# Kernel tuning notes

Measured on AMD Instinct MI355X. Metric: run time of the kernel, lower is better.

Reference implementation:

```python
import jax, jax.numpy as jnp
import numpy as np

BW_MIN, BW_MAX, FLOAT_AMT, NEG_SLOPE = 0.1, 0.5, 0.1, 0.1


def setup_inputs() -> dict:
    key = jax.random.key(0)
    ks = jax.random.split(key, 24)
    B, S, IN_CH, GRID_CH, IC, DIR, OUT_CH = 8, 2000, 120, 64, 512, 4, 2
    NUM_BLOCK = 8
    n_layers = NUM_BLOCK - 2  # 6
    # grid coordinates: meshgrid over [0,10) with gap 0.1 -> 100x100 = 10000 pts
    gx = np.arange(0.0, 10.0, 0.1)
    gy = np.arange(0.0, 10.0, 0.1)
    GX, GY = np.meshgrid(gx, gy)
    grid_coors_xy = jnp.asarray(np.stack([GX.flatten(), GY.flatten()], axis=1), dtype=jnp.float32)  # [N,2]
    N = grid_coors_xy.shape[0]
    cat_ch = IN_CH + 2 * GRID_CH  # 248
    inp = {
        'input_stuff': jax.random.normal(ks[0], (B, S, IN_CH), jnp.float32),
        'sound_loc': jax.random.uniform(ks[1], (B, 4), jnp.float32) * 10.0,  # inside grid extent
        'grid_coors_xy': grid_coors_xy,
        'xy_offset': jnp.zeros((N, 2), jnp.float32),
        'bandwidths': jnp.full((N,), 0.25, jnp.float32),
        'grid_0': jax.random.normal(ks[2], (N, GRID_CH), jnp.float32) / np.sqrt(float(GRID_CH)),
        'proj_W': jax.random.normal(ks[3], (cat_ch, IC), jnp.float32) / np.sqrt(float(cat_ch)),
        'proj_b': jnp.zeros((IC,), jnp.float32),
        'res_W0': jax.random.normal(ks[4], (cat_ch, IC), jnp.float32) / np.sqrt(float(cat_ch)),
        'res_b0': jnp.zeros((IC,), jnp.float32),
        'res_W1': jax.random.normal(ks[5], (IC, IC), jnp.float32) / np.sqrt(float(IC)),
        'res_b1': jnp.zeros((IC,), jnp.float32),
        'layers_W': jax.random.normal(ks[6], (n_layers, IC, IC), jnp.float32) / np.sqrt(float(IC)),
        'layers_b': jnp.zeros((n_layers, IC), jnp.float32),
        'channels': jax.random.normal(ks[7], (NUM_BLOCK - 1, DIR, IC), jnp.float32) / np.sqrt(float(IC)),
        'out_W': jax.random.normal(ks[8], (IC, OUT_CH), jnp.float32) / np.sqrt(float(IC)),
        'out_b': jnp.zeros((OUT_CH,), jnp.float32),
    }
    return inp


def _leaky(x):
    return jax.nn.leaky_relu(x, NEG_SLOPE)


def _fit_predict(grid_pos, grid_feat, query_pos, bandwidths):
    d2 = jnp.sum((query_pos[:, None, :] - grid_pos[None, :, :]) ** 2, axis=-1)  # [B,N]
    w = jnp.exp(-d2 / (bandwidths[None, :] ** 2))                               # [B,N]
    w = w / jnp.sum(w, axis=-1, keepdims=True)
    return w @ grid_feat                                                        # [B,F]


def reference(input_stuff, sound_loc, grid_coors_xy, xy_offset, bandwidths, grid_0,
              proj_W, proj_b, res_W0, res_b0, res_W1, res_b1,
              layers_W, layers_b, channels, out_W, out_b):
    B, S = input_stuff.shape[0], input_stuff.shape[1]
    bw = jnp.clip(bandwidths, BW_MIN, BW_MAX)
    grid_baseline = grid_coors_xy + jnp.tanh(xy_offset) * FLOAT_AMT
    feat0 = _fit_predict(grid_baseline, grid_0, sound_loc[:, :2], bw)  # [B,64]
    feat1 = _fit_predict(grid_baseline, grid_0, sound_loc[:, 2:], bw)  # [B,64]
    total_grid = jnp.concatenate([feat0, feat1], axis=-1)              # [B,128]
    total_grid = jnp.broadcast_to(total_grid[:, None, :], (B, S, total_grid.shape[-1]))
    my_input = jnp.concatenate([total_grid, input_stuff], axis=-1)     # [B,S,248]

    # proj then broadcast over direction channels + learned channel embedding
    out = (my_input @ proj_W + proj_b)[:, :, None, :] + channels[0][None, None]  # [B,S,4,512]

    n_layers = layers_W.shape[0]
    half = n_layers // 2 - 1
    for k in range(n_layers):
        out = _leaky(out) @ layers_W[k] + layers_b[k] + channels[k + 1][None, None]
        if k == half:
            r = _leaky(my_input @ res_W0 + res_b0) @ res_W1 + res_b1  # [B,S,512]
            out = out + r[:, :, None, :]
    return out @ out_W + out_b  # [B,S,4,2]
```

## Files before the change

### kernel.cpp

```cpp
#include <hip/hip_runtime.h>
#include <hip/hip_bf16.h>

#define BB 8
#define SS 2000
#define IN_CH 120
#define GRID_CH 64
#define NPTS 10000
#define IC 512
#define DIRS 4
#define CATCH 248
#define CATPAD 256
#define NLAY 6
#define MROWS 16000
#define MROWS4 64000
#define NSLICE 16
#define PTS_PER_SLICE 625

typedef __bf16 bf16x8 __attribute__((ext_vector_type(8)));
typedef float f32x4 __attribute__((ext_vector_type(4)));

#define DEVI __device__ __forceinline__

DEVI unsigned short f2bf(float f) {
    __hip_bfloat16 h = __float2bfloat16(f);
    return __builtin_bit_cast(unsigned short, h);
}
DEVI float bf2f(unsigned short u) {
    unsigned int x = ((unsigned int)u) << 16;
    return __builtin_bit_cast(float, x);
}
DEVI float leaky(float x) { return x > 0.f ? x : 0.1f * x; }

DEVI void gload16(const void* g, void* l) {
    __builtin_amdgcn_global_load_lds(
        (const unsigned int __attribute__((address_space(1)))*)g,
        (unsigned int __attribute__((address_space(3)))*)l, 16, 0, 0);
}

DEVI int xcd_swizzle() {
    int nwg = (int)gridDim.x;
    int orig = (int)blockIdx.x;
    int q = nwg >> 3, r = nwg & 7;
    int xcd = orig & 7, pos = orig >> 3;
    int base = xcd < r ? xcd * (q + 1) : r * (q + 1) + (xcd - r) * q;
    return base + pos;
}

static const size_t OFF_FEATS  = 0;
static const size_t OFF_PROJWT = 4096;
static const size_t OFF_RES0WT = 266240;
static const size_t OFF_RES1WT = 528384;
static const size_t OFF_LAYWT  = 1052672;
static const size_t OFF_MYIN   = 4198400;
static const size_t OFF_R0     = 12390400;
static const size_t OFF_R      = 28774400;
static const size_t OFF_A0     = 45158400;
static const size_t OFF_A1     = 110694400;

__global__ void wconv_k(const float* __restrict__ src, unsigned short* __restrict__ dst,
                        int K, int Kpad, int N, int total) {
    int idx = blockIdx.x * 256 + threadIdx.x;
    if (idx >= total) return;
    int k = idx % Kpad;
    int rem = idx / Kpad;
    int n = rem % N;
    int l = rem / N;
    float v = (k < K) ? src[((size_t)l * K + k) * N + n] : 0.f;
    dst[idx] = f2bf(v);
}

__global__ __launch_bounds__(256) void feats_part_k(
    const float* __restrict__ gxy, const float* __restrict__ goff,
    const float* __restrict__ bws, const float* __restrict__ g0,
    const float* __restrict__ sloc, float* __restrict__ partial) {
    int bq = blockIdx.x;
    int b = bq >> 1, q = bq & 1;
    float qx = sloc[b * 4 + q * 2 + 0];
    float qy = sloc[b * 4 + q * 2 + 1];
    int i0 = blockIdx.y * PTS_PER_SLICE;
    int iend = i0 + PTS_PER_SLICE;
    float swt = 0.f;
    float sf[64];
#pragma unroll
    for (int c = 0; c < 64; c++) sf[c] = 0.f;
    for (int i = i0 + threadIdx.x; i < iend; i += 256) {
        float gx = gxy[i * 2 + 0] + tanhf(goff[i * 2 + 0]) * 0.1f;
        float gy = gxy[i * 2 + 1] + tanhf(goff[i * 2 + 1]) * 0.1f;
        float bw = fminf(fmaxf(bws[i], 0.1f), 0.5f);
        float dx = qx - gx, dy = qy - gy;
        float w = expf(-(dx * dx + dy * dy) / (bw * bw));
        swt += w;
#pragma unroll
        for (int c = 0; c < 64; c++) sf[c] += w * g0[(size_t)i * 64 + c];
    }
#pragma unroll
    for (int c = 0; c < 64; c++)
        for (int o = 32; o; o >>= 1) sf[c] += __shfl_down(sf[c], o);
    for (int o = 32; o; o >>= 1) swt += __shfl_down(swt, o);
    __shared__ float red[4][65];
    int lane = threadIdx.x & 63, wv = threadIdx.x >> 6;
    if (lane == 0) {
#pragma unroll
        for (int c = 0; c < 64; c++) red[wv][c] = sf[c];
        red[wv][64] = swt;
    }
    __syncthreads();
    size_t base = (size_t)(blockIdx.y * 16 + bq) * 72;
    if (threadIdx.x < 64) {
        int c = threadIdx.x;
        partial[base + c] = red[0][c] + red[1][c] + red[2][c] + red[3][c];
        if (c == 0)
            partial[base + 64] = red[0][64] + red[1][64] + red[2][64] + red[3][64];
    }
}

__global__ __launch_bounds__(128) void feats_reduce_k(
    const float* __restrict__ partial, float* __restrict__ feats) {
    int bq = blockIdx.x;
    __shared__ float s[66];
    int t = threadIdx.x;
    if (t < 65) {
        float acc = 0.f;
        for (int sl = 0; sl < NSLICE; ++sl)
            acc += partial[(size_t)(sl * 16 + bq) * 72 + t];
        s[t] = acc;
    }
    __syncthreads();
    if (t < 64) {
        int b = bq >> 1, q = bq & 1;
        feats[b * 128 + q * 64 + t] = s[t] / s[64];
    }
}

__global__ void build_k(const float* __restrict__ feats, const float* __restrict__ inp,
                        unsigned short* __restrict__ dst) {
    int idx = blockIdx.x * 256 + threadIdx.x;
    int c = idx & 255;
    int m = idx >> 8;
    int b = m / SS;
    float v;
    if (c < 128) v = feats[b * 128 + c];
    else if (c < CATCH) v = inp[(size_t)m * IN_CH + (c - 128)];
    else v = 0.f;
    dst[idx] = f2bf(v);
}

template <int EPI>
__global__ __launch_bounds__(256) void gemm_k(
    const unsigned short* __restrict__ A, const unsigned short* __restrict__ BT,
    unsigned short* __restrict__ out, int K,
    const float* __restrict__ bias, const float* __restrict__ chan,
    const unsigned short* __restrict__ resid) {
    __shared__ __align__(16) unsigned short lds[2][2][8192];
    const int tid = threadIdx.x;
    const int lane = tid & 63, wv = tid >> 6;
    const int wm = wv >> 1, wn = wv & 1;
    const int c8 = lane >> 4;
    const int fr = lane & 15;

    const int swz = xcd_swizzle();
    const int bx = swz >> 2, by = swz & 3;

    int aoff[4][2], boff[4][2];
#pragma unroll
    for (int i = 0; i < 4; i++) {
        int ra = wm * 64 + i * 16 + fr;
        int rb = wn * 64 + i * 16 + fr;
#pragma unroll
        for (int h = 0; h < 2; h++) {
            int c = c8 + h * 4;
            aoff[i][h] = ra * 64 + ((c ^ (ra & 7)) << 3);
            boff[i][h] = rb * 64 + ((c ^ (rb & 7)) << 3);
        }
    }
    int ldso[4];
    size_t asrc[4];
    const unsigned short* Ab = A + (size_t)bx * 128 * K;
    const unsigned short* Bb = BT + (size_t)by * 128 * K;
#pragma unroll
    for (int t = 0; t < 4; t++) {
        int o = t * 4096 + wv * 1024 + lane * 16;
        int r = o >> 7;
        int s = (o >> 4) & 7;
        int g = (s ^ (r & 7)) << 3;
        ldso[t] = o >> 1;
        asrc[t] = (size_t)r * K + g;
    }

    f32x4 acc[4][4];
#pragma unroll
    for (int i = 0; i < 4; i++)
#pragma unroll
        for (int j = 0; j < 4; j++) acc[i][j] = (f32x4)0.f;

    const int nK = K >> 6;
#pragma unroll
    for (int t = 0; t < 4; t++) gload16(Ab + asrc[t], &lds[0][0][ldso[t]]);
#pragma unroll
    for (int t = 0; t < 4; t++) gload16(Bb + asrc[t], &lds[0][1][ldso[t]]);
    asm volatile("s_waitcnt vmcnt(0)" ::: "memory");
    __builtin_amdgcn_s_barrier();
    __builtin_amdgcn_sched_barrier(0);

    int buf = 0;
    for (int kt = 0; kt < nK; ++kt) {
        if (kt + 1 < nK) {
            const int k1 = (kt + 1) << 6;
#pragma unroll
            for (int t = 0; t < 4; t++) gload16(Ab + asrc[t] + k1, &lds[buf ^ 1][0][ldso[t]]);
#pragma unroll
            for (int t = 0; t < 4; t++) gload16(Bb + asrc[t] + k1, &lds[buf ^ 1][1][ldso[t]]);
        }
#pragma unroll
        for (int h = 0; h < 2; h++) {
            bf16x8 av[4], bv[4];
#pragma unroll
            for (int i = 0; i < 4; i++) av[i] = *(const bf16x8*)&lds[buf][0][aoff[i][h]];
#pragma unroll
            for (int j = 0; j < 4; j++) bv[j] = *(const bf16x8*)&lds[buf][1][boff[j][h]];
#pragma unroll
            for (int i = 0; i < 4; i++)
#pragma unroll
                for (int j = 0; j < 4; j++)
                    acc[i][j] = __builtin_amdgcn_mfma_f32_16x16x32_bf16(av[i], bv[j], acc[i][j], 0, 0, 0);
        }
        if (kt + 1 < nK) {
            asm volatile("s_waitcnt vmcnt(0)" ::: "memory");
            __builtin_amdgcn_s_barrier();
            __builtin_amdgcn_sched_barrier(0);
        }
        buf ^= 1;
    }

    const int rbase = (lane >> 4) << 2;
    const size_t m0 = (size_t)bx * 128;
    const int n0 = by * 128;
#pragma unroll
    for (int i = 0; i < 4; i++) {
#pragma unroll
        for (int j = 0; j < 4; j++) {
#pragma unroll
            for (int rg = 0; rg < 4; ++rg) {
                size_t m = m0 + wm * 64 + i * 16 + rbase + rg;
                int n = n0 + wn * 64 + j * 16 + fr;
                float v = acc[i][j][rg];
                if constexpr (EPI == 0) {
                    float v0 = v + bias[n];
#pragma unroll
                    for (int d = 0; d < 4; ++d) {
                        float u = v0 + chan[d * 512 + n];
                        out[(m * 4 + d) * 512 + n] = f2bf(leaky(u));
                    }
                } else if constexpr (EPI == 1 || EPI == 2 || EPI == 3) {
                    int d = (int)(m & 3);
                    float u = v + bias[n] + chan[d * 512 + n];
                    if constexpr (EPI == 2) u += bf2f(resid[(m >> 2) * 512 + n]);
                    out[m * 512 + n] = f2bf(EPI == 3 ? u : leaky(u));
                } else {
                    float u = v + bias[n];
                    out[m * 512 + n] = f2bf(EPI == 4 ? leaky(u) : u);
                }
            }
        }
    }
}

__global__ __launch_bounds__(256) void final_k(
    const unsigned short* __restrict__ A, const float* __restrict__ outW,
    const float* __restrict__ outb, float* __restrict__ out) {
    int gw = blockIdx.x * 4 + (threadIdx.x >> 6);
    int lane = threadIdx.x & 63;
    const unsigned short* row = A + (size_t)gw * 512;
    uint4 bits = *(const uint4*)(row + lane * 8);
    unsigned int ww[4] = {bits.x, bits.y, bits.z, bits.w};
    float s0 = 0.f, s1 = 0.f;
#pragma unroll
    for (int j = 0; j < 8; j++) {
        unsigned short u = (unsigned short)((ww[j >> 1] >> ((j & 1) * 16)) & 0xffff);
        float a = bf2f(u);
        int k = lane * 8 + j;
        s0 = fmaf(a, outW[k * 2 + 0], s0);
        s1 = fmaf(a, outW[k * 2 + 1], s1);
    }
    for (int o = 32; o; o >>= 1) {
        s0 += __shfl_down(s0, o);
        s1 += __shfl_down(s1, o);
    }
    if (lane == 0) {
        out[(size_t)gw * 2 + 0] = s0 + outb[0];
        out[(size_t)gw * 2 + 1] = s1 + outb[1];
    }
}

extern "C" void kernel_launch(void* const* d_in, const int* in_sizes, int n_in,
                              void* d_out, int out_size, void* d_ws, size_t ws_size,
                              hipStream_t stream) {
    const float* input_stuff = (const float*)d_in[0];
    const float* sound_loc   = (const float*)d_in[1];
    const float* grid_xy     = (const float*)d_in[2];
    const float* xy_offset   = (const float*)d_in[3];
    const float* bandwidths  = (const float*)d_in[4];
    const float* grid_0      = (const float*)d_in[5];
    const float* proj_W      = (const float*)d_in[6];
    const float* proj_b      = (const float*)d_in[7];
    const float* res_W0      = (const float*)d_in[8];
    const float* res_b0      = (const float*)d_in[9];
    const float* res_W1      = (const float*)d_in[10];
    const float* res_b1      = (const float*)d_in[11];
    const float* layers_W    = (const float*)d_in[12];
    const float* layers_b    = (const float*)d_in[13];
    const float* channels    = (const float*)d_in[14];
    const float* out_W       = (const float*)d_in[15];
    const float* out_b       = (const float*)d_in[16];

    char* ws = (char*)d_ws;
    float* feats            = (float*)(ws + OFF_FEATS);
    unsigned short* projWT  = (unsigned short*)(ws + OFF_PROJWT);
    unsigned short* res0WT  = (unsigned short*)(ws + OFF_RES0WT);
    unsigned short* res1WT  = (unsigned short*)(ws + OFF_RES1WT);
    unsigned short* layWT   = (unsigned short*)(ws + OFF_LAYWT);
    unsigned short* myin    = (unsigned short*)(ws + OFF_MYIN);
    unsigned short* R0      = (unsigned short*)(ws + OFF_R0);
    unsigned short* Rb      = (unsigned short*)(ws + OFF_R);
    unsigned short* A0      = (unsigned short*)(ws + OFF_A0);
    unsigned short* A1      = (unsigned short*)(ws + OFF_A1);
    float* partial          = (float*)(ws + OFF_A0);

    wconv_k<<<(512 * 256 + 255) / 256, 256, 0, stream>>>(proj_W, projWT, CATCH, CATPAD, IC, 512 * 256);
    wconv_k<<<(512 * 256 + 255) / 256, 256, 0, stream>>>(res_W0, res0WT, CATCH, CATPAD, IC, 512 * 256);
    wconv_k<<<(512 * 512 + 255) / 256, 256, 0, stream>>>(res_W1, res1WT, IC, IC, IC, 512 * 512);
    wconv_k<<<(6 * 512 * 512 + 255) / 256, 256, 0, stream>>>(layers_W, layWT, IC, IC, IC, 6 * 512 * 512);

    feats_part_k<<<dim3(16, NSLICE), 256, 0, stream>>>(grid_xy, xy_offset, bandwidths, grid_0, sound_loc, partial);
    feats_reduce_k<<<16, 128, 0, stream>>>(partial, feats);
    build_k<<<MROWS, 256, 0, stream>>>(feats, input_stuff, myin);

    gemm_k<0><<<500, 256, 0, stream>>>(myin, projWT, A0, CATPAD, proj_b, channels, nullptr);
    gemm_k<4><<<500, 256, 0, stream>>>(myin, res0WT, R0, CATPAD, res_b0, nullptr, nullptr);
    gemm_k<5><<<500, 256, 0, stream>>>(R0, res1WT, Rb, IC, res_b1, nullptr, nullptr);
    gemm_k<1><<<2000, 256, 0, stream>>>(A0, layWT + 0 * 262144, A1, IC, layers_b + 0 * 512, channels + 1 * 2048, nullptr);
    gemm_k<1><<<2000, 256, 0, stream>>>(A1, layWT + 1 * 262144, A0, IC, layers_b + 1 * 512, channels + 2 * 2048, nullptr);
    gemm_k<2><<<2000, 256, 0, stream>>>(A0, layWT + 2 * 262144, A1, IC, layers_b + 2 * 512, channels + 3 * 2048, Rb);
    gemm_k<1><<<2000, 256, 0, stream>>>(A1, layWT + 3 * 262144, A0, IC, layers_b + 3 * 512, channels + 4 * 2048, nullptr);
    gemm_k<1><<<2000, 256, 0, stream>>>(A0, layWT + 4 * 262144, A1, IC, layers_b + 4 * 512, channels + 5 * 2048, nullptr);
    gemm_k<3><<<2000, 256, 0, stream>>>(A1, layWT + 5 * 262144, A0, IC, layers_b + 5 * 512, channels + 6 * 2048, nullptr);

    final_k<<<MROWS, 256, 0, stream>>>(A0, out_W, out_b, (float*)d_out);
}
```

Baseline: 403.8 us.

## Halve GEMM K-tile to 32 with k-chunk-major LDS layout and higher occupancy

Shrinks the GEMM K-step from 64 to 32, halving LDS from 64KB to 32KB per block. The LDS layout changes from row-major with XOR swizzle to k-chunk-major, so fragment reads need no swizzle. Launch bounds now request 4 blocks per CU to improve latency hiding. In exchange there are twice as many K iterations and barriers, and each sync has less MFMA work to hide global load latency behind.

```diff
diff --git a/kernel.cpp b/kernel.cpp
--- a/kernel.cpp
+++ b/kernel.cpp
@@ -4,13 +4,10 @@
 #define BB 8
 #define SS 2000
 #define IN_CH 120
-#define GRID_CH 64
 #define NPTS 10000
 #define IC 512
-#define DIRS 4
 #define CATCH 248
 #define CATPAD 256
-#define NLAY 6
 #define MROWS 16000
 #define MROWS4 64000
 #define NSLICE 16
@@ -146,12 +143,12 @@
 }
 
 template <int EPI>
-__global__ __launch_bounds__(256) void gemm_k(
+__global__ __launch_bounds__(256, 4) void gemm_k(
     const unsigned short* __restrict__ A, const unsigned short* __restrict__ BT,
     unsigned short* __restrict__ out, int K,
     const float* __restrict__ bias, const float* __restrict__ chan,
     const unsigned short* __restrict__ resid) {
-    __shared__ __align__(16) unsigned short lds[2][2][8192];
+    __shared__ __align__(16) unsigned short lds[2][2][4096];
     const int tid = threadIdx.x;
     const int lane = tid & 63, wv = tid >> 6;
     const int wm = wv >> 1, wn = wv & 1;
@@ -161,30 +158,23 @@
     const int swz = xcd_swizzle();
     const int bx = swz >> 2, by = swz & 3;
 
-    int aoff[4][2], boff[4][2];
+    int aoff[4], boff[4];
 #pragma unroll
     for (int i = 0; i < 4; i++) {
-        int ra = wm * 64 + i * 16 + fr;
-        int rb = wn * 64 + i * 16 + fr;
-#pragma unroll
-        for (int h = 0; h < 2; h++) {
-            int c = c8 + h * 4;
-            aoff[i][h] = ra * 64 + ((c ^ (ra & 7)) << 3);
-            boff[i][h] = rb * 64 + ((c ^ (rb & 7)) << 3);
-        }
-    }
-    int ldso[4];
-    size_t asrc[4];
+        aoff[i] = c8 * 1024 + (wm * 64 + i * 16 + fr) * 8;
+        boff[i] = c8 * 1024 + (wn * 64 + i * 16 + fr) * 8;
+    }
+    int ldso[2];
+    size_t src[2];
     const unsigned short* Ab = A + (size_t)bx * 128 * K;
     const unsigned short* Bb = BT + (size_t)by * 128 * K;
 #pragma unroll
-    for (int t = 0; t < 4; t++) {
-        int o = t * 4096 + wv * 1024 + lane * 16;
-        int r = o >> 7;
-        int s = (o >> 4) & 7;
-        int g = (s ^ (r & 7)) << 3;
+    for (int t = 0; t < 2; t++) {
+        int o = t * 4096 + tid * 16;
+        int ck = o >> 11;
+        int r = (o >> 4) & 127;
         ldso[t] = o >> 1;
-        asrc[t] = (size_t)r * K + g;
+        src[t] = (size_t)r * K + ck * 8;
     }
 
     f32x4 acc[4][4];
@@ -193,11 +183,11 @@
 #pragma unroll
         for (int j = 0; j < 4; j++) acc[i][j] = (f32x4)0.f;
 
-    const int nK = K >> 6;
-#pragma unroll
-    for (int t = 0; t < 4; t++) gload16(Ab + asrc[t], &lds[0][0][ldso[t]]);
-#pragma unroll
-    for (int t = 0; t < 4; t++) gload16(Bb + asrc[t], &lds[0][1][ldso[t]]);
+    const int nK = K >> 5;
+#pragma unroll
+    for (int t = 0; t < 2; t++) gload16(Ab + src[t], &lds[0][0][ldso[t]]);
+#pragma unroll
+    for (int t = 0; t < 2; t++) gload16(Bb + src[t], &lds[0][1][ldso[t]]);
     asm volatile("s_waitcnt vmcnt(0)" ::: "memory");
     __builtin_amdgcn_s_barrier();
     __builtin_amdgcn_sched_barrier(0);
@@ -205,25 +195,22 @@
     int buf = 0;
     for (int kt = 0; kt < nK; ++kt) {
         if (kt + 1 < nK) {
-            const int k1 = (kt + 1) << 6;
-#pragma unroll
-            for (int t = 0; t < 4; t++) gload16(Ab + asrc[t] + k1, &lds[buf ^ 1][0][ldso[t]]);
-#pragma unroll
-            for (int t = 0; t < 4; t++) gload16(Bb + asrc[t] + k1, &lds[buf ^ 1][1][ldso[t]]);
+            const int k1 = (kt + 1) << 5;
+#pragma unroll
+            for (int t = 0; t < 2; t++) gload16(Ab + src[t] + k1, &lds[buf ^ 1][0][ldso[t]]);
+#pragma unroll
+            for (int t = 0; t < 2; t++) gload16(Bb + src[t] + k1, &lds[buf ^ 1][1][ldso[t]]);
         }
-#pragma unroll
-        for (int h = 0; h < 2; h++) {
-            bf16x8 av[4], bv[4];
-#pragma unroll
-            for (int i = 0; i < 4; i++) av[i] = *(const bf16x8*)&lds[buf][0][aoff[i][h]];
-#pragma unroll
-            for (int j = 0; j < 4; j++) bv[j] = *(const bf16x8*)&lds[buf][1][boff[j][h]];
-#pragma unroll
-            for (int i = 0; i < 4; i++)
-#pragma unroll
-                for (int j = 0; j < 4; j++)
-                    acc[i][j] = __builtin_amdgcn_mfma_f32_16x16x32_bf16(av[i], bv[j], acc[i][j], 0, 0, 0);
-        }
+        bf16x8 av[4], bv[4];
+#pragma unroll
+        for (int i = 0; i < 4; i++) av[i] = *(const bf16x8*)&lds[buf][0][aoff[i]];
+#pragma unroll
+        for (int j = 0; j < 4; j++) bv[j] = *(const bf16x8*)&lds[buf][1][boff[j]];
+#pragma unroll
+        for (int i = 0; i < 4; i++)
+#pragma unroll
+            for (int j = 0; j < 4; j++)
+                acc[i][j] = __builtin_amdgcn_mfma_f32_16x16x32_bf16(av[i], bv[j], acc[i][j], 0, 0, 0);
         if (kt + 1 < nK) {
             asm volatile("s_waitcnt vmcnt(0)" ::: "memory");
             __builtin_amdgcn_s_barrier();
```

Result: slower. 596.7 us (+47.8%).
